# Kernel tuning notes

Measured on AMD Instinct MI355X. Metric: run time of the kernel, lower is better.

Reference implementation:

```python
import jax, jax.numpy as jnp
import numpy as np

B, N, D, E = 16, 64, 512, 512
MSG = 512          # message_size must equal edge_feature_size (scatter into edge states)
LINK_H = 512       # GraphConv hidden channels
P = 2              # propagate_layers
HOI, ROLES = 26, 2


def setup_inputs() -> dict:
    key = jax.random.key(0)
    ks = jax.random.split(key, 12)
    s = 0.02
    return dict(
        edge_features=jax.random.normal(ks[0], (B, N, N, E), jnp.float32),
        node_features=jax.random.normal(ks[1], (B, N, D), jnp.float32),
        node_labels=jnp.zeros((B, N, HOI), jnp.float32),
        node_roles=jnp.zeros((B, N, ROLES), jnp.float32),
        # message_fun 'linear_concat_relu': Linear(D+E -> MSG) + ReLU
        Wm=(jax.random.normal(ks[2], (MSG, D + E), jnp.float32) * s),
        bm=jnp.zeros((MSG,), jnp.float32),
        # link_fun GraphConv: 1x1 Conv2d stack E->LINK_H->LINK_H->1
        Wl1=(jax.random.normal(ks[3], (LINK_H, E), jnp.float32) * s),
        bl1=jnp.zeros((LINK_H,), jnp.float32),
        Wl2=(jax.random.normal(ks[4], (LINK_H, LINK_H), jnp.float32) * s),
        bl2=jnp.zeros((LINK_H,), jnp.float32),
        Wlo=(jax.random.normal(ks[5], (1, LINK_H), jnp.float32) * s),
        blo=jnp.zeros((1,), jnp.float32),
        # update_fun GRU(input=MSG, hidden=D), torch gate order r,z,n
        W_ih=(jax.random.normal(ks[6], (3 * D, MSG), jnp.float32) * s),
        b_ih=jnp.zeros((3 * D,), jnp.float32),
        W_hh=(jax.random.normal(ks[7], (3 * D, D), jnp.float32) * s),
        b_hh=jnp.zeros((3 * D,), jnp.float32),
        # readout FCs
        Wr1=(jax.random.normal(ks[8], (HOI, D), jnp.float32) * s),
        br1=jnp.zeros((HOI,), jnp.float32),
        Wr2=(jax.random.normal(ks[9], (ROLES, D), jnp.float32) * s),
        br2=jnp.zeros((ROLES,), jnp.float32),
    )


def _link(x, Wl1, bl1, Wl2, bl2, Wlo, blo):
    # x: [B, C, N, N]; 1x1 conv stack -> [B, N, N]
    h = jax.nn.relu(jnp.einsum('bcvw,hc->bhvw', x, Wl1) + bl1[None, :, None, None])
    h = jax.nn.relu(jnp.einsum('bcvw,hc->bhvw', h, Wl2) + bl2[None, :, None, None])
    return (jnp.einsum('bcvw,hc->bhvw', h, Wlo) + blo[None, :, None, None])[:, 0]


def _forward(edge_features, node_features, Wm, bm, Wl1, bl1, Wl2, bl2, Wlo, blo,
             W_ih, b_ih, W_hh, b_hh, Wr1, br1, Wr2, br2):
    e = jnp.transpose(edge_features, (0, 3, 1, 2))   # [B,E,v,w]
    nf = jnp.transpose(node_features, (0, 2, 1))     # [B,D,N]
    # hidden node states are never written back in the source, so raw messages
    # m(h_w, e_vw) are constant across propagation rounds: compute once, vectorized over v.
    h_part = jnp.broadcast_to(nf[:, :, None, :], (B, D, N, N))   # h_w broadcast over v
    cat = jnp.concatenate([h_part, e], axis=1)                   # [B, D+E, v, w]
    M = jax.nn.relu(jnp.einsum('bcvw,mc->bmvw', cat, Wm) + bm[None, :, None, None])
    edge_state = e
    gated = M
    for _ in range(P):
        pred_adj = _link(edge_state, Wl1, bl1, Wl2, bl2, Wlo, blo)      # [B,v,w]
        gated = jax.nn.sigmoid(pred_adj)[:, None, :, :] * M            # [B,m,v,w]
        # source stores m_v into hidden_edge_states[..., :, :, i_node] (column v)
        edge_state = jnp.swapaxes(gated, 2, 3)
    m_sum = jnp.sum(gated, axis=3)                   # [B, m, v]
    x = jnp.swapaxes(m_sum, 1, 2)                    # [B, N, MSG] GRU input
    h = node_features                                # [B, N, D]  GRU hidden
    gi = x @ W_ih.T + b_ih
    gh = h @ W_hh.T + b_hh
    ir, iz, inn = jnp.split(gi, 3, axis=-1)
    hr, hz, hn = jnp.split(gh, 3, axis=-1)
    r = jax.nn.sigmoid(ir + hr)
    z = jax.nn.sigmoid(iz + hz)
    n = jnp.tanh(inn + r * hn)
    h_new = (1.0 - z) * n + z * h
    pred_node_labels = h_new @ Wr1.T + br1
    pred_node_roles = h_new @ Wr2.T + br2
    return pred_adj, pred_node_labels, pred_node_roles


def reference(edge_features, node_features, node_labels, node_roles, Wm, bm,
              Wl1, bl1, Wl2, bl2, Wlo, blo, W_ih, b_ih, W_hh, b_hh,
              Wr1, br1, Wr2, br2):
    return _forward(edge_features, node_features, Wm, bm, Wl1, bl1, Wl2, bl2,
                    Wlo, blo, W_ih, b_ih, W_hh, b_hh, Wr1, br1, Wr2, br2)
```

## Files before the change

kernel.cpp:

```cpp
#include <hip/hip_runtime.h>
#include <hip/hip_bf16.h>
#include <stdint.h>
#include <stddef.h>


using u16 = unsigned short;
using u32 = unsigned int;

__device__ __forceinline__ float u2f(u16 u) {
  union { unsigned i; float f; } c; c.i = ((unsigned)u) << 16; return c.f;
}
__device__ __forceinline__ u16 f2u(float f) {
  __hip_bfloat16 h = __float2bfloat16(f);
  union { __hip_bfloat16 h; u16 u; } c; c.h = h; return c.u;
}
__device__ __forceinline__ u32 pk2(float lo, float hi) {
  __hip_bfloat162 h = __float22bfloat162_rn(make_float2(lo, hi));
  union { __hip_bfloat162 h; u32 u; } c; c.h = h; return c.u;
}
__device__ __forceinline__ float sigm(float x) { return 1.f / (1.f + expf(-x)); }

typedef __attribute__((ext_vector_type(8))) short bfrag;
typedef __attribute__((ext_vector_type(4))) float f32x4;

__device__ __forceinline__ void gl_lds16(const u16* g, u16* l) {
  __builtin_amdgcn_global_load_lds((const __attribute__((address_space(1))) void*)g,
                                   (__attribute__((address_space(3))) void*)l,
                                   16, 0, 0);
}

#define NSEG 17
struct CvtArgs {
  const float* src[NSEG];
  u16* dst[NSEG];
  int cum[NSEG + 1];
};
__global__ __launch_bounds__(256) void cvt_multi(CvtArgs a, int total) {
  int i = blockIdx.x * 256 + threadIdx.x;
  if (i >= total) return;
  int s = 0;
  while (s + 1 < NSEG && i >= a.cum[s + 1]) ++s;
  const int off = i - a.cum[s];
  a.dst[s][off] = f2u(a.src[s][off]);
}

template <int MODE, bool A32>
__global__ __launch_bounds__(256)
void gemm_bt(const void* __restrict__ Av, int lda, size_t abase,
             const u16* __restrict__ W, int ldw, int K,
             const u16* __restrict__ bias,
             const float* __restrict__ ubuf,
             const u16* __restrict__ wlo,
             float* __restrict__ pred,
             u16* __restrict__ outb,
             float* __restrict__ outf,
             int ldc,
             const u16* __restrict__ W2, int ldw2, u16* __restrict__ outb2)
{
  __shared__ u16 smem[32768];
  u16* const Abase = smem;
  u16* const Bbase = smem + 16384;

  const int tid  = threadIdx.x;
  const int wave = tid >> 6, lane = tid & 63;
  const int wr = wave >> 1, wc = wave & 1;
  const int quad = lane >> 4, l16 = lane & 15;
  const int srow8 = lane >> 3;
  const int scolsw = ((lane & 7) ^ srow8) * 8;

  const int gx = gridDim.x;
  const int nwg = gx * gridDim.y;
  int flat = blockIdx.y * gx + blockIdx.x;
  if ((nwg & 7) == 0) { const int q = nwg >> 3; flat = (flat & 7) * q + (flat >> 3); }
  const int bx = flat % gx;
  const int by = flat / gx;

  const int row0 = by * 128;
  const bool isM = (MODE != 5) || (bx < 4);
  const int col0 = (MODE == 5 ? (bx & 3) : bx) * 128;
  const u16* Wp  = (MODE == 5 && !isM) ? W2  : W;
  const int ldwp = (MODE == 5 && !isM) ? ldw2 : ldw;

  f32x4 acc[4][4];
#pragma unroll
  for (int i = 0; i < 4; i++)
#pragma unroll
    for (int j = 0; j < 4; j++)
#pragma unroll
      for (int r = 0; r < 4; r++) acc[i][j][r] = 0.f;

  float4 rf[8];
  uint4  ra[4];

  auto stageA = [&](int kk0, u16* dst) {
#pragma unroll
    for (int i = 0; i < 4; i++) {
      const int chunk = wave * 4 + i;
      gl_lds16((const u16*)Av + (abase + (size_t)(row0 + chunk * 8 + srow8)) * lda + kk0 + scolsw,
               dst + chunk * 512 + lane * 8);
    }
  };
  auto stageB = [&](int kk0, u16* dst) {
#pragma unroll
    for (int i = 0; i < 4; i++) {
      const int chunk = wave * 4 + i;
      gl_lds16(Wp + (size_t)(col0 + chunk * 8 + srow8) * ldwp + kk0 + scolsw,
               dst + chunk * 512 + lane * 8);
    }
  };
  auto loadRF = [&](int kk0) {
#pragma unroll
    for (int i = 0; i < 4; i++) {
      const int idx = i * 256 + tid, sr = idx >> 3, sc = (idx & 7) * 8;
      const float* p = (const float*)Av + (abase + (size_t)(row0 + sr)) * lda + kk0 + sc;
      rf[2 * i]     = *(const float4*)p;
      rf[2 * i + 1] = *(const float4*)(p + 4);
    }
  };
  auto convRA = [&]() {
#pragma unroll
    for (int i = 0; i < 4; i++) {
      ra[i].x = pk2(rf[2 * i].x, rf[2 * i].y);
      ra[i].y = pk2(rf[2 * i].z, rf[2 * i].w);
      ra[i].z = pk2(rf[2 * i + 1].x, rf[2 * i + 1].y);
      ra[i].w = pk2(rf[2 * i + 1].z, rf[2 * i + 1].w);
    }
  };
  auto writeA = [&](u16* dst) {
#pragma unroll
    for (int i = 0; i < 4; i++) {
      const int idx = i * 256 + tid, sr = idx >> 3, cb = idx & 7;
      *(uint4*)(dst + sr * 64 + ((cb ^ (sr & 7)) << 3)) = ra[i];
    }
  };
  auto compute = [&](const u16* Ac, const u16* Bc) {
#pragma unroll
    for (int kk = 0; kk < 64; kk += 32) {
      const int cb0 = (kk >> 3) + quad;
      const int cbsw = ((cb0 ^ (l16 & 7)) << 3);
      bfrag af[4], bf[4];
#pragma unroll
      for (int mt = 0; mt < 4; mt++) {
        const int R = wr * 64 + mt * 16 + l16;
        af[mt] = *(const bfrag*)(Ac + R * 64 + cbsw);
      }
#pragma unroll
      for (int nt2 = 0; nt2 < 4; nt2++) {
        const int R = wc * 64 + nt2 * 16 + l16;
        bf[nt2] = *(const bfrag*)(Bc + R * 64 + cbsw);
      }
#pragma unroll
      for (int mt = 0; mt < 4; mt++)
#pragma unroll
        for (int nt2 = 0; nt2 < 4; nt2++)
          acc[mt][nt2] = __builtin_amdgcn_mfma_f32_16x16x32_bf16(af[mt], bf[nt2], acc[mt][nt2], 0, 0, 0);
    }
  };

  const int ntile = K >> 6;
  int cur = 0;

  if constexpr (A32) {
    loadRF(0); convRA(); writeA(Abase);
    stageB(0, Bbase);
    if (ntile > 1) loadRF(64);
  } else {
    stageA(0, Abase);
    stageB(0, Bbase);
  }
  __syncthreads();

  for (int t = 0; t < ntile; ++t) {
    const bool more = (t + 1 < ntile);
    u16* Ac = Abase + cur * 8192;
    u16* Bc = Bbase + cur * 8192;
    u16* An = Abase + (cur ^ 1) * 8192;
    u16* Bn = Bbase + (cur ^ 1) * 8192;
    if (more) {
      if constexpr (!A32) stageA((t + 1) << 6, An);
      stageB((t + 1) << 6, Bn);
    }
    compute(Ac, Bc);
    if constexpr (A32) {
      if (more) {
        convRA(); writeA(An);
        if (t + 2 < ntile) loadRF((t + 2) << 6);
      }
    }
    __syncthreads();
    cur ^= 1;
  }

  if constexpr (MODE == 2) {
#pragma unroll
    for (int mt = 0; mt < 4; mt++) {
#pragma unroll
      for (int r = 0; r < 4; r++) {
        const int rg = row0 + wr * 64 + mt * 16 + quad * 4 + r;
        float s = 0.f;
#pragma unroll
        for (int nt = 0; nt < 4; nt++) {
          const int cg = col0 + wc * 64 + nt * 16 + l16;
          float v = acc[mt][nt][r] + u2f(bias[cg]);
          v = fmaxf(v, 0.f);
          s += v * u2f(wlo[cg]);
        }
#pragma unroll
        for (int off = 1; off < 16; off <<= 1) s += __shfl_xor(s, off, 16);
        if (l16 == 0) atomicAdd(pred + rg, s);
      }
    }
  } else if constexpr (MODE == 3) {
#pragma unroll
    for (int mt = 0; mt < 4; mt++)
#pragma unroll
      for (int nt = 0; nt < 4; nt++)
#pragma unroll
        for (int r = 0; r < 4; r++) {
          const int rg = row0 + wr * 64 + mt * 16 + quad * 4 + r;
          const int cg = col0 + wc * 64 + nt * 16 + l16;
          outf[(size_t)rg * ldc + cg] = acc[mt][nt][r] + u2f(bias[cg]);
        }
  } else {
    u16* tile = smem;
    u16* outp = (MODE == 5 && !isM) ? outb2 : outb;
    __syncthreads();
#pragma unroll
    for (int mt = 0; mt < 4; mt++)
#pragma unroll
      for (int nt = 0; nt < 4; nt++)
#pragma unroll
        for (int r = 0; r < 4; r++) {
          const int lrow = wr * 64 + mt * 16 + quad * 4 + r;
          const int lcol = wc * 64 + nt * 16 + l16;
          const int rg = row0 + lrow;
          const int cg = col0 + lcol;
          float v = acc[mt][nt][r];
          if (MODE == 0 || (MODE == 5 && isM)) {
            const size_t grow = abase + rg;
            const int urow = (int)(((grow >> 12) << 6) | (grow & 63));
            v += ubuf[(size_t)urow * 512 + cg];
            v = fmaxf(v, 0.f);
          } else if (MODE == 1 || MODE == 5) {
            v += u2f(bias[cg]);
            v = fmaxf(v, 0.f);
          } else {
            v = sigm(pred[rg]) * v + u2f(bias[cg]);
            v = fmaxf(v, 0.f);
          }
          tile[lrow * 136 + lcol] = f2u(v);
        }
    __syncthreads();
    const int row = tid >> 1, half = tid & 1;
    const u16* src = tile + row * 136 + half * 64;
    u16* dst = outp + (size_t)(row0 + row) * ldc + col0 + half * 64;
#pragma unroll
    for (int j = 0; j < 8; j++)
      *(uint4*)(dst + j * 8) = *(const uint4*)(src + j * 8);
  }
}

__global__ void fill_kernel(float* __restrict__ p, const u16* __restrict__ val, int n) {
  int i = blockIdx.x * blockDim.x + threadIdx.x;
  if (i < n) p[i] = u2f(*val);
}

__global__ void adj_out_kernel(const float* __restrict__ r, float* __restrict__ out) {
  int i = blockIdx.x * 256 + threadIdx.x;
  int b = i >> 12, v = (i >> 6) & 63, w = i & 63;
  out[i] = r[(b << 12) + (w << 6) + v];
}

__global__ __launch_bounds__(512)
void msum_kernel(const float* __restrict__ r, const u16* __restrict__ M, u16* __restrict__ x) {
  const int bv = blockIdx.x;
  const int b = bv >> 6, v = bv & 63;
  __shared__ float s[64];
  if (threadIdx.x < 64) {
    const int w = threadIdx.x;
    s[w] = sigm(r[(b << 12) + (w << 6) + v]);
  }
  __syncthreads();
  const int m = threadIdx.x;
  const u16* Mp = M + (((size_t)(b << 12) + (v << 6)) << 9) + m;
  float acc = 0.f;
#pragma unroll 8
  for (int w = 0; w < 64; w++) acc += s[w] * u2f(Mp[(size_t)w << 9]);
  x[(size_t)bv * 512 + m] = f2u(acc);
}

__global__ __launch_bounds__(256)
void gru_kernel(const float* __restrict__ gi, const float* __restrict__ gh,
                const u16* __restrict__ h, float* __restrict__ hn) {
  int i = blockIdx.x * 256 + threadIdx.x;
  int row = i >> 9, d = i & 511;
  const float* gir = gi + (size_t)row * 1536;
  const float* ghr = gh + (size_t)row * 1536;
  float rr = sigm(gir[d] + ghr[d]);
  float z  = sigm(gir[512 + d] + ghr[512 + d]);
  float n  = tanhf(gir[1024 + d] + rr * ghr[1024 + d]);
  float hv = u2f(h[i]);
  hn[i] = (1.f - z) * n + z * hv;
}

__global__ __launch_bounds__(256)
void readout_kernel(const float* __restrict__ hn,
                    const u16* __restrict__ Wr1, const u16* __restrict__ br1,
                    const u16* __restrict__ Wr2, const u16* __restrict__ br2,
                    float* __restrict__ out) {
  const int row = blockIdx.x;
  __shared__ float hrow[512];
  for (int d = threadIdx.x; d < 512; d += 256) hrow[d] = hn[(size_t)row * 512 + d];
  __syncthreads();
  const int wave = threadIdx.x >> 6, lane = threadIdx.x & 63;
  for (int j = wave; j < 28; j += 4) {
    const u16* wrow;
    float bias;
    size_t off;
    if (j < 26) { wrow = Wr1 + (size_t)j * 512; bias = u2f(br1[j]); off = 65536 + (size_t)row * 26 + j; }
    else { int jj = j - 26; wrow = Wr2 + (size_t)jj * 512; bias = u2f(br2[jj]); off = 92160 + (size_t)row * 2 + jj; }
    float s = 0.f;
    for (int d = lane; d < 512; d += 64) s += hrow[d] * u2f(wrow[d]);
#pragma unroll
    for (int o = 32; o; o >>= 1) s += __shfl_down(s, o);
    if (lane == 0) out[off] = s + bias;
  }
}

extern "C" void kernel_launch(void* const* d_in, const int* in_sizes, int n_in,
                              void* d_out, int out_size, void* d_ws, size_t ws_size,
                              hipStream_t stream)
{
  (void)in_sizes; (void)n_in; (void)out_size;
  const void*  X  = d_in[0];
  char* ws = (char*)d_ws;

  const bool big = (ws_size >= 158905344ULL);

  u16 *Mb, *H1, *xb, *nfb, *Wmb, *bmb, *Wl1b, *bl1b, *Wl2b, *bl2b, *Wlob, *blob;
  u16 *Wihb, *bihb, *Whhb, *bhhb, *Wr1b, *br1b, *Wr2b, *br2b;
  float *pred1, *rbuf, *ubuf, *gi, *gh, *hn;
  if (big) {
    Mb    = (u16*)(ws);
    H1    = (u16*)(ws + 67108864);
    pred1 = (float*)(ws + 134217728);
    rbuf  = (float*)(ws + 134479872);
    ubuf  = (float*)(ws + 134742016);
    xb    = (u16*)(ws + 136839168);
    gi    = (float*)(ws + 137887744);
    gh    = (float*)(ws + 144179200);
    hn    = (float*)(ws + 150470656);
    nfb   = (u16*)(ws + 152567808);
    Wmb   = (u16*)(ws + 153616384);
    bmb   = (u16*)(ws + 154664960);
    Wl1b  = (u16*)(ws + 154665984);
    bl1b  = (u16*)(ws + 155190272);
    Wl2b  = (u16*)(ws + 155191296);
    bl2b  = (u16*)(ws + 155715584);
    Wlob  = (u16*)(ws + 155716608);
    blob  = (u16*)(ws + 155717632);
    Wihb  = (u16*)(ws + 155718656);
    bihb  = (u16*)(ws + 157291520);
    Whhb  = (u16*)(ws + 157295616);
    bhhb  = (u16*)(ws + 158868480);
    Wr1b  = (u16*)(ws + 158872576);
    br1b  = (u16*)(ws + 158901248);
    Wr2b  = (u16*)(ws + 158902272);
    br2b  = (u16*)(ws + 158904320);
  } else {
    Mb    = (u16*)(ws);
    H1    = (u16*)(ws + 67108864);
    pred1 = (float*)(ws + 83886080);
    rbuf  = (float*)(ws + 84148224);
    ubuf  = (float*)(ws + 84410368);
    xb    = (u16*)(ws + 86507520);
    gi    = (float*)(ws + 87556096);
    gh    = (float*)(ws + 93847552);
    hn    = (float*)(ws + 100139008);
    nfb   = (u16*)(ws + 102236416);
    Wmb   = (u16*)(ws + 103284992);
    bmb   = (u16*)(ws + 104333568);
    Wl1b  = (u16*)(ws + 104334592);
    bl1b  = (u16*)(ws + 104858880);
    Wl2b  = (u16*)(ws + 104859904);
    bl2b  = (u16*)(ws + 105384192);
    Wlob  = (u16*)(ws + 105385216);
    blob  = (u16*)(ws + 105386240);
    Wihb  = (u16*)(ws + 105387264);
    bihb  = (u16*)(ws + 106960128);
    Whhb  = (u16*)(ws + 106964224);
    bhhb  = (u16*)(ws + 108537088);
    Wr1b  = (u16*)(ws + 108541184);
    br1b  = (u16*)(ws + 108573952);
    Wr2b  = (u16*)(ws + 108574976);
    br2b  = (u16*)(ws + 108579072);
  }

  float* out = (float*)d_out;

  {
    CvtArgs ca;
    const int seg_in[NSEG]  = {1,4,5,6,7,8,9,10,11,12,13,14,15,16,17,18,19};
    u16* seg_dst[NSEG] = {nfb,Wmb,bmb,Wl1b,bl1b,Wl2b,bl2b,Wlob,blob,
                          Wihb,bihb,Whhb,bhhb,Wr1b,br1b,Wr2b,br2b};
    const int seg_n[NSEG] = {524288,524288,512,262144,512,262144,512,512,1,
                             786432,1536,786432,1536,13312,26,1024,2};
    int total = 0;
    for (int s = 0; s < NSEG; s++) {
      ca.src[s] = (const float*)d_in[seg_in[s]];
      ca.dst[s] = seg_dst[s];
      ca.cum[s] = total;
      total += seg_n[s];
    }
    ca.cum[NSEG] = total;
    cvt_multi<<<(total + 255) / 256, 256, 0, stream>>>(ca, total);
  }

  gemm_bt<3, false><<<dim3(4, 8), 256, 0, stream>>>(nfb, 512, 0, Wmb, 1024, 512, bmb,
      nullptr, nullptr, nullptr, nullptr, ubuf, 512, nullptr, 0, nullptr);
  fill_kernel<<<512, 256, 0, stream>>>(pred1, blob, 131072);

  if (big) {
    gemm_bt<5, true><<<dim3(8, 512), 256, 0, stream>>>(X, 512, 0, Wmb + 512, 1024, 512,
        bl1b, ubuf, nullptr, nullptr, Mb, nullptr, 512, Wl1b, 512, H1);
    gemm_bt<2, false><<<dim3(4, 512), 256, 0, stream>>>(H1, 512, 0, Wl2b, 512, 512, bl2b,
        nullptr, Wlob, pred1, nullptr, nullptr, 512, nullptr, 0, nullptr);
    gemm_bt<4, false><<<dim3(4, 512), 256, 0, stream>>>(Mb, 512, 0, Wl1b, 512, 512, bl1b,
        nullptr, nullptr, pred1, H1, nullptr, 512, nullptr, 0, nullptr);
    gemm_bt<2, false><<<dim3(4, 512), 256, 0, stream>>>(H1, 512, 0, Wl2b, 512, 512, bl2b,
        nullptr, Wlob, rbuf, nullptr, nullptr, 512, nullptr, 0, nullptr);
  } else {
    gemm_bt<0, true><<<dim3(4, 512), 256, 0, stream>>>(X, 512, 0, Wmb + 512, 1024, 512,
        nullptr, ubuf, nullptr, nullptr, Mb, nullptr, 512, nullptr, 0, nullptr);
    for (int q = 0; q < 4; q++) {
      const size_t ro = (size_t)q * 16384;
      gemm_bt<1, true><<<dim3(4, 128), 256, 0, stream>>>(X, 512, ro, Wl1b, 512, 512, bl1b,
          nullptr, nullptr, nullptr, H1, nullptr, 512, nullptr, 0, nullptr);
      gemm_bt<2, false><<<dim3(4, 128), 256, 0, stream>>>(H1, 512, 0, Wl2b, 512, 512, bl2b,
          nullptr, Wlob, pred1 + ro, nullptr, nullptr, 512, nullptr, 0, nullptr);
    }
    for (int q = 0; q < 4; q++) {
      const size_t ro = (size_t)q * 16384;
      gemm_bt<4, false><<<dim3(4, 128), 256, 0, stream>>>(Mb, 512, ro, Wl1b, 512, 512, bl1b,
          nullptr, nullptr, pred1 + ro, H1, nullptr, 512, nullptr, 0, nullptr);
      gemm_bt<2, false><<<dim3(4, 128), 256, 0, stream>>>(H1, 512, 0, Wl2b, 512, 512, bl2b,
          nullptr, Wlob, rbuf + ro, nullptr, nullptr, 512, nullptr, 0, nullptr);
    }
  }

  adj_out_kernel<<<256, 256, 0, stream>>>(rbuf, out);
  msum_kernel<<<1024, 512, 0, stream>>>(rbuf, Mb, xb);
  gemm_bt<3, false><<<dim3(12, 8), 256, 0, stream>>>(xb, 512, 0, Wihb, 512, 512, bihb,
      nullptr, nullptr, nullptr, nullptr, gi, 1536, nullptr, 0, nullptr);
  gemm_bt<3, false><<<dim3(12, 8), 256, 0, stream>>>(nfb, 512, 0, Whhb, 512, 512, bhhb,
      nullptr, nullptr, nullptr, nullptr, gh, 1536, nullptr, 0, nullptr);
  gru_kernel<<<2048, 256, 0, stream>>>(gi, gh, nfb, hn);
  readout_kernel<<<1024, 256, 0, stream>>>(hn, Wr1b, br1b, Wr2b, br2b, out);
}
```

Before: 661.7 us.

## Add 256x256-tile 512-thread GEMM kernel for the big edge-path GEMMs

Adds a new gemm256 kernel with 256x256 output tiles, 512 threads (8 waves in a 2x4 grid), K-step 32, double-buffered LDS and an XCD-aware block remap. The four large edge GEMMs in the big path now use it. Larger tiles raise arithmetic intensity and cut how often A and B are re-read from global memory, at the cost of high register pressure from 128 accumulator floats per thread. The old kernel also moves the fp32 A conversion/write ahead of compute.

Measured after the change: 696.9 us. +5.3%, slower.

```diff
diff --git a/kernel.cpp b/kernel.cpp
--- a/kernel.cpp
+++ b/kernel.cpp
@@ -42,6 +42,213 @@
   while (s + 1 < NSEG && i >= a.cum[s + 1]) ++s;
   const int off = i - a.cum[s];
   a.dst[s][off] = f2u(a.src[s][off]);
+}
+
+template <int MODE, bool A32>
+__global__ __launch_bounds__(512, 2)
+void gemm256(const void* __restrict__ Av, int lda, size_t abase,
+             const u16* __restrict__ W, int ldw, int K,
+             const u16* __restrict__ bias,
+             const float* __restrict__ ubuf,
+             const u16* __restrict__ wlo,
+             float* __restrict__ pred,
+             u16* __restrict__ outb, int ldc,
+             const u16* __restrict__ W2, int ldw2, u16* __restrict__ outb2)
+{
+  __shared__ u16 smem[32768];
+  u16* const As0 = smem;
+  u16* const Bs0 = smem + 8192;
+  u16* const As1 = smem + 16384;
+  u16* const Bs1 = smem + 24576;
+
+  const int tid  = threadIdx.x;
+  const int wave = tid >> 6, lane = tid & 63;
+  const int wr = wave >> 2, wc = wave & 3;
+  const int quad = lane >> 4, l16 = lane & 15;
+  const int swz = (quad ^ ((l16 >> 1) & 3)) << 3;
+
+  const int gx = gridDim.x;
+  const int nwg = gx * gridDim.y;
+  int flat = blockIdx.y * gx + blockIdx.x;
+  if ((nwg & 7) == 0) { const int q = nwg >> 3; flat = (flat & 7) * q + (flat >> 3); }
+  const int bx = flat % gx;
+  const int by = flat / gx;
+
+  const int row0 = by * 256;
+  const bool isM = (MODE != 5) || (bx < 2);
+  const int col0 = (MODE == 5 ? (bx & 1) : bx) * 256;
+  const u16* Wp  = (MODE == 5 && !isM) ? W2  : W;
+  const int ldwp = (MODE == 5 && !isM) ? ldw2 : ldw;
+
+  f32x4 acc[8][4];
+#pragma unroll
+  for (int i = 0; i < 8; i++)
+#pragma unroll
+    for (int j = 0; j < 4; j++)
+#pragma unroll
+      for (int r = 0; r < 4; r++) acc[i][j][r] = 0.f;
+
+  auto stageB = [&](int k0, u16* Bb) {
+#pragma unroll
+    for (int p = 0; p < 2; p++) {
+      const int idx = p * 512 + tid;
+      const int row = idx >> 2;
+      const int cb  = (idx & 3) ^ ((row >> 1) & 3);
+      gl_lds16(Wp + (size_t)(col0 + row) * ldwp + k0 + cb * 8, Bb + idx * 8);
+    }
+  };
+  auto stageA = [&](int k0, u16* Ab) {
+#pragma unroll
+    for (int p = 0; p < 2; p++) {
+      const int idx = p * 512 + tid;
+      const int row = idx >> 2;
+      const int cb  = (idx & 3) ^ ((row >> 1) & 3);
+      gl_lds16((const u16*)Av + (abase + (size_t)(row0 + row)) * lda + k0 + cb * 8,
+               Ab + idx * 8);
+    }
+  };
+
+  float4 rfa[2][4];
+
+#define LOADRF(k0, S) {                                                          \
+    const float* p_ = (const float*)Av +                                         \
+        (abase + (size_t)(row0 + (tid >> 1))) * lda + (k0) + (tid & 1) * 16;     \
+    rfa[S][0] = *(const float4*)p_;      rfa[S][1] = *(const float4*)(p_ + 4);   \
+    rfa[S][2] = *(const float4*)(p_ + 8); rfa[S][3] = *(const float4*)(p_ + 12); }
+
+#define WRITEA(S, Ab) {                                                          \
+    const int r_ = tid >> 1, h_ = tid & 1;                                       \
+    const int sw_ = (r_ >> 1) & 3;                                               \
+    uint4 w0_, w1_;                                                              \
+    w0_.x = pk2(rfa[S][0].x, rfa[S][0].y); w0_.y = pk2(rfa[S][0].z, rfa[S][0].w);\
+    w0_.z = pk2(rfa[S][1].x, rfa[S][1].y); w0_.w = pk2(rfa[S][1].z, rfa[S][1].w);\
+    w1_.x = pk2(rfa[S][2].x, rfa[S][2].y); w1_.y = pk2(rfa[S][2].z, rfa[S][2].w);\
+    w1_.z = pk2(rfa[S][3].x, rfa[S][3].y); w1_.w = pk2(rfa[S][3].z, rfa[S][3].w);\
+    *(uint4*)((Ab) + r_ * 32 + (((2 * h_) ^ sw_) << 3))     = w0_;               \
+    *(uint4*)((Ab) + r_ * 32 + (((2 * h_ + 1) ^ sw_) << 3)) = w1_; }
+
+  auto compute = [&](const u16* Ab, const u16* Bb) {
+    bfrag af[8], bf[4];
+#pragma unroll
+    for (int mt = 0; mt < 8; mt++)
+      af[mt] = *(const bfrag*)(Ab + wr * 4096 + mt * 512 + l16 * 32 + swz);
+#pragma unroll
+    for (int nt = 0; nt < 4; nt++)
+      bf[nt] = *(const bfrag*)(Bb + wc * 2048 + nt * 512 + l16 * 32 + swz);
+#pragma unroll
+    for (int mt = 0; mt < 8; mt++)
+#pragma unroll
+      for (int nt = 0; nt < 4; nt++)
+        acc[mt][nt] = __builtin_amdgcn_mfma_f32_16x16x32_bf16(af[mt], bf[nt], acc[mt][nt], 0, 0, 0);
+  };
+
+  const int ntile = K >> 5;
+
+  if constexpr (A32) {
+    LOADRF(0, 0);
+    WRITEA(0, As0);
+    stageB(0, Bs0);
+    if (ntile > 1) LOADRF(32, 1);
+  } else {
+    stageA(0, As0);
+    stageB(0, Bs0);
+  }
+  __syncthreads();
+
+  for (int t = 0; t < ntile; t += 2) {
+    {
+      const bool more = (t + 1 < ntile);
+      if (more) {
+        stageB((t + 1) << 5, Bs1);
+        if constexpr (!A32) stageA((t + 1) << 5, As1);
+        if constexpr (A32) {
+          WRITEA(1, As1);
+          if (t + 2 < ntile) LOADRF((t + 2) << 5, 0);
+        }
+      }
+      compute(As0, Bs0);
+      __syncthreads();
+    }
+    if (t + 1 < ntile) {
+      const bool more = (t + 2 < ntile);
+      if (more) {
+        stageB((t + 2) << 5, Bs0);
+        if constexpr (!A32) stageA((t + 2) << 5, As0);
+        if constexpr (A32) {
+          WRITEA(0, As0);
+          if (t + 3 < ntile) LOADRF((t + 3) << 5, 1);
+        }
+      }
+      compute(As1, Bs1);
+      __syncthreads();
+    }
+  }
+#undef LOADRF
+#undef WRITEA
+
+  if constexpr (MODE == 2) {
+#pragma unroll
+    for (int mt = 0; mt < 8; mt++) {
+#pragma unroll
+      for (int r = 0; r < 4; r++) {
+        const int rg = row0 + wr * 128 + mt * 16 + quad * 4 + r;
+        float s = 0.f;
+#pragma unroll
+        for (int nt = 0; nt < 4; nt++) {
+          const int cg = col0 + wc * 64 + nt * 16 + l16;
+          float v = acc[mt][nt][r] + u2f(bias[cg]);
+          v = fmaxf(v, 0.f);
+          s += v * u2f(wlo[cg]);
+        }
+#pragma unroll
+        for (int off = 1; off < 16; off <<= 1) s += __shfl_xor(s, off, 16);
+        if (l16 == 0) atomicAdd(pred + rg, s);
+      }
+    }
+  } else {
+    u16* outp = (MODE == 5 && !isM) ? outb2 : outb;
+    u16* tile = smem;
+#pragma unroll
+    for (int p = 0; p < 4; p++) {
+      __syncthreads();
+      if (wr == (p >> 1)) {
+        const int mtb = (p & 1) * 4;
+#pragma unroll
+        for (int mi = 0; mi < 4; mi++) {
+          const int mt = mtb + mi;
+#pragma unroll
+          for (int nt = 0; nt < 4; nt++)
+#pragma unroll
+            for (int r = 0; r < 4; r++) {
+              const int rg = row0 + wr * 128 + mt * 16 + quad * 4 + r;
+              const int cg = col0 + wc * 64 + nt * 16 + l16;
+              float v = acc[mt][nt][r];
+              if (MODE == 5 && isM) {
+                const size_t grow = (size_t)rg;
+                const int urow = (int)(((grow >> 12) << 6) | (grow & 63));
+                v += ubuf[(size_t)urow * 512 + cg];
+                v = fmaxf(v, 0.f);
+              } else if (MODE == 5) {
+                v += u2f(bias[cg]);
+                v = fmaxf(v, 0.f);
+              } else {
+                v = sigm(pred[rg]) * v + u2f(bias[cg]);
+                v = fmaxf(v, 0.f);
+              }
+              const int lrow = mt * 16 + quad * 4 + r - (p & 1) * 64;
+              tile[lrow * 264 + wc * 64 + nt * 16 + l16] = f2u(v);
+            }
+        }
+      }
+      __syncthreads();
+      const int row = tid >> 3, ch = tid & 7;
+      const u16* src = tile + row * 264 + ch * 32;
+      u16* dst = outp + (size_t)(row0 + p * 64 + row) * ldc + col0 + ch * 32;
+#pragma unroll
+      for (int j = 0; j < 4; j++)
+        *(uint4*)(dst + j * 8) = *(const uint4*)(src + j * 8);
+    }
+  }
 }
 
 template <int MODE, bool A32>
@@ -179,14 +386,12 @@
     if (more) {
       if constexpr (!A32) stageA((t + 1) << 6, An);
       stageB((t + 1) << 6, Bn);
-    }
-    compute(Ac, Bc);
-    if constexpr (A32) {
-      if (more) {
+      if constexpr (A32) {
         convRA(); writeA(An);
         if (t + 2 < ntile) loadRF((t + 2) << 6);
       }
     }
+    compute(Ac, Bc);
     __syncthreads();
     cur ^= 1;
   }
@@ -421,14 +626,14 @@
   fill_kernel<<<512, 256, 0, stream>>>(pred1, blob, 131072);
 
   if (big) {
-    gemm_bt<5, true><<<dim3(8, 512), 256, 0, stream>>>(X, 512, 0, Wmb + 512, 1024, 512,
-        bl1b, ubuf, nullptr, nullptr, Mb, nullptr, 512, Wl1b, 512, H1);
-    gemm_bt<2, false><<<dim3(4, 512), 256, 0, stream>>>(H1, 512, 0, Wl2b, 512, 512, bl2b,
-        nullptr, Wlob, pred1, nullptr, nullptr, 512, nullptr, 0, nullptr);
-    gemm_bt<4, false><<<dim3(4, 512), 256, 0, stream>>>(Mb, 512, 0, Wl1b, 512, 512, bl1b,
-        nullptr, nullptr, pred1, H1, nullptr, 512, nullptr, 0, nullptr);
-    gemm_bt<2, false><<<dim3(4, 512), 256, 0, stream>>>(H1, 512, 0, Wl2b, 512, 512, bl2b,
-        nullptr, Wlob, rbuf, nullptr, nullptr, 512, nullptr, 0, nullptr);
+    gemm256<5, true><<<dim3(4, 256), 512, 0, stream>>>(X, 512, 0, Wmb + 512, 1024, 512,
+        bl1b, ubuf, nullptr, nullptr, Mb, 512, Wl1b, 512, H1);
+    gemm256<2, false><<<dim3(2, 256), 512, 0, stream>>>(H1, 512, 0, Wl2b, 512, 512, bl2b,
+        nullptr, Wlob, pred1, nullptr, 512, nullptr, 0, nullptr);
+    gemm256<4, false><<<dim3(2, 256), 512, 0, stream>>>(Mb, 512, 0, Wl1b, 512, 512, bl1b,
+        nullptr, nullptr, pred1, H1, 512, nullptr, 0, nullptr);
+    gemm256<2, false><<<dim3(2, 256), 512, 0, stream>>>(H1, 512, 0, Wl2b, 512, 512, bl2b,
+        nullptr, Wlob, rbuf, nullptr, 512, nullptr, 0, nullptr);
   } else {
     gemm_bt<0, true><<<dim3(4, 512), 256, 0, stream>>>(X, 512, 0, Wmb + 512, 1024, 512,
         nullptr, ubuf, nullptr, nullptr, Mb, nullptr, 512, nullptr, 0, nullptr);
```
